# Performance work log

Measured on AMD Instinct MI355X. Metric: run time of the kernel, lower is better.

The kernel has to match this reference:

```python
import jax, jax.numpy as jnp
import numpy as np

EMBED_DIM = 768
HEAD_SIZE = 64

def setup_inputs() -> dict:
    key = jax.random.key(0)
    k1, k2, k3, k4 = jax.random.split(key, 4)
    x = jax.random.normal(k1, (4, 4096, EMBED_DIM), dtype=jnp.float32)
    # nn.Linear(E, H, bias=False) weights, stored as [E, H] for y = x @ W
    scale = 1.0 / np.sqrt(EMBED_DIM)
    Wk = jax.random.uniform(k2, (EMBED_DIM, HEAD_SIZE), jnp.float32, -scale, scale)
    Wq = jax.random.uniform(k3, (EMBED_DIM, HEAD_SIZE), jnp.float32, -scale, scale)
    Wv = jax.random.uniform(k4, (EMBED_DIM, HEAD_SIZE), jnp.float32, -scale, scale)
    return {"x": x, "Wk": Wk, "Wq": Wq, "Wv": Wv}

def reference(x, Wk, Wq, Wv):
    # x: [B, S, E]
    E = x.shape[2]
    K = jnp.einsum("bse,eh->bsh", x, Wk)  # [B, S, H]
    Q = jnp.einsum("bse,eh->bsh", x, Wq)
    V = jnp.einsum("bse,eh->bsh", x, Wv)
    # NOTE: original scales by embedding_dim**0.5, not head_size**0.5
    A = jnp.einsum("bqh,bkh->bqk", Q, K) / jnp.sqrt(jnp.asarray(E, x.dtype))
    A = jax.nn.softmax(A, axis=-1)
    # dropout is inference-mode identity
    return jnp.einsum("bqk,bkh->bqh", A, V)
```

## Files before the change

kernel.cpp:

```cpp
#include <hip/hip_runtime.h>

typedef __attribute__((ext_vector_type(8))) short short8;
typedef __attribute__((ext_vector_type(4))) short short4v;
typedef __attribute__((ext_vector_type(4))) float float4v;

__device__ __forceinline__ short f2bf(float f) {
    union { float f; unsigned u; } v; v.f = f;
    return (short)((v.u + 0x7fffu + ((v.u >> 16) & 1u)) >> 16);
}

__device__ __forceinline__ float fast_exp2(float x) {
#if __has_builtin(__builtin_amdgcn_exp2f)
    return __builtin_amdgcn_exp2f(x);
#else
    return exp2f(x);
#endif
}

__global__ void wtrans_kernel(const float* __restrict__ Wk, const float* __restrict__ Wq,
                              const float* __restrict__ Wv, short* __restrict__ Wt3) {
    int idx = blockIdx.x * 256 + threadIdx.x;
    int j = idx / (64 * 768);
    int rem = idx - j * (64 * 768);
    int n = rem / 768, k = rem - n * 768;
    const float* W = (j == 0) ? Wq : (j == 1 ? Wk : Wv);
    float scale = (j == 0) ? 0.05205877f : 1.0f;
    Wt3[idx] = f2bf(W[k * 64 + n] * scale);
}

__global__ __launch_bounds__(256, 4) void proj_kernel(
    const float* __restrict__ x, const short* __restrict__ Wt3,
    short* __restrict__ Qs, short* __restrict__ Kb, short* __restrict__ Vtr)
{
    __shared__ alignas(16) float red[3 * 64 * 48];
    const int tid = threadIdx.x;
    const int wave = tid >> 6, lane = tid & 63, quad = lane >> 4, l16 = lane & 15;
    const int m0 = blockIdx.x * 16;
    const int kb = wave * 192;
    const float* xr = x + (size_t)(m0 + l16) * 768 + kb + quad * 8;

    float4v acc[3][4];
#pragma unroll
    for (int j = 0; j < 3; ++j)
#pragma unroll
        for (int nt = 0; nt < 4; ++nt) acc[j][nt] = (float4v){0.f, 0.f, 0.f, 0.f};

#pragma unroll
    for (int it = 0; it < 6; ++it) {
        float4 u0 = *(const float4*)(xr + it * 32);
        float4 u1 = *(const float4*)(xr + it * 32 + 4);
        short8 a;
        a[0] = f2bf(u0.x); a[1] = f2bf(u0.y); a[2] = f2bf(u0.z); a[3] = f2bf(u0.w);
        a[4] = f2bf(u1.x); a[5] = f2bf(u1.y); a[6] = f2bf(u1.z); a[7] = f2bf(u1.w);
        const short* wb = Wt3 + kb + it * 32 + quad * 8;
#pragma unroll
        for (int j = 0; j < 3; ++j)
#pragma unroll
            for (int nt = 0; nt < 4; ++nt) {
                short8 bf = *(const short8*)(wb + (size_t)(j * 64 + nt * 16 + l16) * 768);
                acc[j][nt] = __builtin_amdgcn_mfma_f32_16x16x32_bf16(a, bf, acc[j][nt], 0, 0, 0);
            }
    }

    if (wave != 0) {
        float* dst = &red[((wave - 1) * 64 + lane) * 48];
#pragma unroll
        for (int j = 0; j < 3; ++j)
#pragma unroll
            for (int nt = 0; nt < 4; ++nt)
                *(float4v*)(dst + (j * 4 + nt) * 4) = acc[j][nt];
    }
    __syncthreads();
    if (wave == 0) {
#pragma unroll
        for (int w = 0; w < 3; ++w) {
            const float* srcp = &red[(w * 64 + lane) * 48];
#pragma unroll
            for (int j = 0; j < 3; ++j)
#pragma unroll
                for (int nt = 0; nt < 4; ++nt)
                    acc[j][nt] += *(const float4v*)(srcp + (j * 4 + nt) * 4);
        }
    }
    __syncthreads();

    short* sm = (short*)red;
    if (wave == 0) {
#pragma unroll
        for (int j = 0; j < 2; ++j) {
            short* dst = (j == 0) ? Qs : Kb;
#pragma unroll
            for (int nt = 0; nt < 4; ++nt)
#pragma unroll
                for (int r = 0; r < 4; ++r)
                    dst[(size_t)(m0 + quad * 4 + r) * 64 + nt * 16 + l16] = f2bf(acc[j][nt][r]);
        }
#pragma unroll
        for (int nt = 0; nt < 4; ++nt)
#pragma unroll
            for (int r = 0; r < 4; ++r)
                sm[(quad * 4 + r) * 72 + nt * 16 + l16] = f2bf(acc[2][nt][r]);
    }
    __syncthreads();
    {
        const int h = tid >> 2, si = (tid & 3) * 4;
        const int b = m0 >> 12, s0 = m0 & 4095;
        short4v tmp;
#pragma unroll
        for (int i = 0; i < 4; ++i) tmp[i] = sm[(si + i) * 72 + h];
        *(short4v*)(Vtr + (size_t)(b * 64 + h) * 4096 + s0 + si) = tmp;
    }
}

__global__ __launch_bounds__(256, 4) void attn_kernel(
    const short* __restrict__ Qs, const short* __restrict__ Kb, const short* __restrict__ Vt,
    float* __restrict__ Opart, float* __restrict__ Ll, int kv_len)
{
    __shared__ alignas(16) short Kl[64 * 72];
    __shared__ alignas(16) short Vl[64 * 72];
    __shared__ alignas(16) short Pl[4 * 32 * 72];

    const int tid = threadIdx.x;
    const int wave = tid >> 6, lane = tid & 63, quad = lane >> 4, l16 = lane & 15;
    const int qt = blockIdx.x, b = blockIdx.y, sp = blockIdx.z;
    const int q0 = qt * 128;
    const int bS = b * 4096;
    const int kv0 = sp * kv_len;

    short8 qa[2][2];
#pragma unroll
    for (int mt = 0; mt < 2; ++mt)
#pragma unroll
        for (int ks = 0; ks < 2; ++ks)
            qa[mt][ks] = *(const short8*)(Qs + (size_t)(bS + q0 + wave * 32 + mt * 16 + l16) * 64 + ks * 32 + quad * 8);

    float4v o[2][4];
    float rs[2][4];
#pragma unroll
    for (int mt = 0; mt < 2; ++mt)
#pragma unroll
        for (int nt = 0; nt < 4; ++nt) o[mt][nt] = (float4v){0.f, 0.f, 0.f, 0.f};
#pragma unroll
    for (int mt = 0; mt < 2; ++mt)
#pragma unroll
        for (int r = 0; r < 4; ++r) rs[mt][r] = 0.f;

    const int sr = tid >> 2, sc = (tid & 3) * 16;
    short* plw = &Pl[wave * 2304];

    for (int kt = 0; kt < kv_len; kt += 64) {
        const int kvg = kv0 + kt;
        __syncthreads();
        {
            const short* src = Kb + (size_t)(bS + kvg + sr) * 64 + sc;
            *(short8*)&Kl[sr * 72 + sc]     = *(const short8*)src;
            *(short8*)&Kl[sr * 72 + sc + 8] = *(const short8*)(src + 8);
            const short* vs = Vt + (size_t)(b * 64 + sr) * 4096 + kvg + sc;
            *(short8*)&Vl[sr * 72 + sc]     = *(const short8*)vs;
            *(short8*)&Vl[sr * 72 + sc + 8] = *(const short8*)(vs + 8);
        }
        __syncthreads();

        float4v s[2][4];
#pragma unroll
        for (int nt = 0; nt < 4; ++nt) {
            short8 b0 = *(const short8*)&Kl[(nt * 16 + l16) * 72 + quad * 8];
            short8 b1 = *(const short8*)&Kl[(nt * 16 + l16) * 72 + 32 + quad * 8];
#pragma unroll
            for (int mt = 0; mt < 2; ++mt) {
                float4v a0 = (float4v){0.f, 0.f, 0.f, 0.f};
                a0 = __builtin_amdgcn_mfma_f32_16x16x32_bf16(qa[mt][0], b0, a0, 0, 0, 0);
                a0 = __builtin_amdgcn_mfma_f32_16x16x32_bf16(qa[mt][1], b1, a0, 0, 0, 0);
                s[mt][nt] = a0;
            }
        }

#pragma unroll
        for (int mt = 0; mt < 2; ++mt)
#pragma unroll
            for (int nt = 0; nt < 4; ++nt)
#pragma unroll
                for (int r = 0; r < 4; ++r) {
                    float p = fast_exp2(s[mt][nt][r]);
                    rs[mt][r] += p;
                    plw[(mt * 16 + quad * 4 + r) * 72 + nt * 16 + l16] = f2bf(p);
                }

#pragma unroll
        for (int ks = 0; ks < 2; ++ks) {
            short8 bf[4];
#pragma unroll
            for (int nt = 0; nt < 4; ++nt)
                bf[nt] = *(const short8*)&Vl[(nt * 16 + l16) * 72 + ks * 32 + quad * 8];
#pragma unroll
            for (int mt = 0; mt < 2; ++mt) {
                short8 af = *(const short8*)&plw[(mt * 16 + l16) * 72 + ks * 32 + quad * 8];
#pragma unroll
                for (int nt = 0; nt < 4; ++nt)
                    o[mt][nt] = __builtin_amdgcn_mfma_f32_16x16x32_bf16(af, bf[nt], o[mt][nt], 0, 0, 0);
            }
        }
    }

#pragma unroll
    for (int mt = 0; mt < 2; ++mt)
#pragma unroll
        for (int r = 0; r < 4; ++r) {
#pragma unroll
            for (int off = 8; off >= 1; off >>= 1)
                rs[mt][r] += __shfl_xor(rs[mt][r], off);
        }

#pragma unroll
    for (int mt = 0; mt < 2; ++mt) {
#pragma unroll
        for (int nt = 0; nt < 4; ++nt)
#pragma unroll
            for (int r = 0; r < 4; ++r) {
                int qb = q0 + wave * 32 + mt * 16 + quad * 4 + r;
                Opart[((size_t)sp * 16384 + bS + qb) * 64 + nt * 16 + l16] = o[mt][nt][r];
            }
        if (l16 == 0) {
#pragma unroll
            for (int r = 0; r < 4; ++r) {
                int qb = q0 + wave * 32 + mt * 16 + quad * 4 + r;
                Ll[(size_t)sp * 16384 + bS + qb] = rs[mt][r];
            }
        }
    }
}

__global__ void combine_kernel(const float* __restrict__ Opart, const float* __restrict__ Ll,
                               float* __restrict__ out, int nsplit) {
    int idx = blockIdx.x * 256 + threadIdx.x;
    int q = idx >> 6;
    float den = 0.f, num = 0.f;
    for (int s = 0; s < nsplit; ++s) {
        den += Ll[s * 16384 + q];
        num += Opart[(size_t)s * 1048576 + idx];
    }
    out[idx] = num / den;
}

extern "C" void kernel_launch(void* const* d_in, const int* in_sizes, int n_in,
                              void* d_out, int out_size, void* d_ws, size_t ws_size,
                              hipStream_t stream) {
    const float* x  = (const float*)d_in[0];
    const float* Wk = (const float*)d_in[1];
    const float* Wq = (const float*)d_in[2];
    const float* Wv = (const float*)d_in[3];
    float* out = (float*)d_out;

    char* w = (char*)d_ws;
    size_t off = 0;
    auto take = [&](size_t bytes) -> void* {
        void* p = w + off;
        off = (off + bytes + 255) & ~(size_t)255;
        return p;
    };
    short* Qs  = (short*)take((size_t)16384 * 64 * 2);
    short* Kb  = (short*)take((size_t)16384 * 64 * 2);
    short* Vt  = (short*)take((size_t)16384 * 64 * 2);
    short* Wt3 = (short*)take((size_t)3 * 64 * 768 * 2);

    size_t base = off;
    int nsplit = 8;
    while (nsplit > 1) {
        size_t need = base + (((size_t)nsplit * 16384 * 4 + 255) & ~(size_t)255)
                      + (size_t)nsplit * 16384 * 64 * 4 + 512;
        if (need <= ws_size) break;
        nsplit >>= 1;
    }
    float* Ll    = (float*)take((size_t)nsplit * 16384 * 4);
    float* Opart = (float*)take((size_t)nsplit * 16384 * 64 * 4);

    wtrans_kernel<<<576, 256, 0, stream>>>(Wk, Wq, Wv, Wt3);
    proj_kernel<<<1024, 256, 0, stream>>>(x, Wt3, Qs, Kb, Vt);
    dim3 ag(32, 4, nsplit);
    attn_kernel<<<ag, 256, 0, stream>>>(Qs, Kb, Vt, Opart, Ll, 4096 / nsplit);
    combine_kernel<<<4096, 256, 0, stream>>>(Opart, Ll, out, nsplit);
}
```

Before: 163.0 us.

## Split projection across output tiles per wave with fragment-ordered weights and prefetch

The projection kernel previously split the K dimension across four waves and reduced partial accumulators through shared memory. Now each wave owns three output 16-column tiles over the full K range, which removes the LDS reduction and its barriers. Weights are pre-permuted into MFMA fragment order so each lane does one contiguous 16-byte load. A three-deep register prefetch of x and weight fragments hides load latency. Each wave now reads the whole x row strip, so x is loaded four times per block from cache instead of once, and the loop is longer.

```diff
diff --git a/kernel.cpp b/kernel.cpp
--- a/kernel.cpp
+++ b/kernel.cpp
@@ -18,88 +18,82 @@
 }
 
 __global__ void wtrans_kernel(const float* __restrict__ Wk, const float* __restrict__ Wq,
-                              const float* __restrict__ Wv, short* __restrict__ Wt3) {
+                              const float* __restrict__ Wv, short* __restrict__ Wt3T) {
     int idx = blockIdx.x * 256 + threadIdx.x;
-    int j = idx / (64 * 768);
-    int rem = idx - j * (64 * 768);
-    int n = rem / 768, k = rem - n * 768;
+    int p = idx / 12288;
+    int rem = idx - p * 12288;
+    int kstep = rem / 512;
+    int r2 = rem - kstep * 512;
+    int lane = r2 >> 3, i = r2 & 7;
+    int quad = lane >> 4, l16 = lane & 15;
+    int j = p >> 2, nt = p & 3;
+    int n = nt * 16 + l16;
+    int k = kstep * 32 + quad * 8 + i;
     const float* W = (j == 0) ? Wq : (j == 1 ? Wk : Wv);
     float scale = (j == 0) ? 0.05205877f : 1.0f;
-    Wt3[idx] = f2bf(W[k * 64 + n] * scale);
-}
-
-__global__ __launch_bounds__(256, 4) void proj_kernel(
-    const float* __restrict__ x, const short* __restrict__ Wt3,
+    Wt3T[idx] = f2bf(W[k * 64 + n] * scale);
+}
+
+__global__ __launch_bounds__(256) void proj_kernel(
+    const float* __restrict__ x, const short* __restrict__ Wt3T,
     short* __restrict__ Qs, short* __restrict__ Kb, short* __restrict__ Vtr)
 {
-    __shared__ alignas(16) float red[3 * 64 * 48];
+    __shared__ alignas(16) short sm[16 * 72];
     const int tid = threadIdx.x;
     const int wave = tid >> 6, lane = tid & 63, quad = lane >> 4, l16 = lane & 15;
     const int m0 = blockIdx.x * 16;
-    const int kb = wave * 192;
-    const float* xr = x + (size_t)(m0 + l16) * 768 + kb + quad * 8;
-
-    float4v acc[3][4];
-#pragma unroll
-    for (int j = 0; j < 3; ++j)
-#pragma unroll
-        for (int nt = 0; nt < 4; ++nt) acc[j][nt] = (float4v){0.f, 0.f, 0.f, 0.f};
-
-#pragma unroll
-    for (int it = 0; it < 6; ++it) {
-        float4 u0 = *(const float4*)(xr + it * 32);
-        float4 u1 = *(const float4*)(xr + it * 32 + 4);
+    const int p0 = wave * 3;
+    const float* xr = x + (size_t)(m0 + l16) * 768 + quad * 8;
+    const short* wt0 = Wt3T + (size_t)(p0 * 24) * 512 + lane * 8;
+
+    float4 X[3][2];
+    short8 Wf[3][3];
+#pragma unroll
+    for (int s = 0; s < 2; ++s) {
+        X[s][0] = *(const float4*)(xr + s * 32);
+        X[s][1] = *(const float4*)(xr + s * 32 + 4);
+#pragma unroll
+        for (int t = 0; t < 3; ++t)
+            Wf[s][t] = *(const short8*)(wt0 + t * 12288 + s * 512);
+    }
+
+    float4v acc[3];
+#pragma unroll
+    for (int t = 0; t < 3; ++t) acc[t] = (float4v){0.f, 0.f, 0.f, 0.f};
+
+#pragma unroll
+    for (int it = 0; it < 24; ++it) {
+        const int cur = it % 3, nxt = (it + 2) % 3;
+        if (it < 22) {
+            X[nxt][0] = *(const float4*)(xr + (it + 2) * 32);
+            X[nxt][1] = *(const float4*)(xr + (it + 2) * 32 + 4);
+#pragma unroll
+            for (int t = 0; t < 3; ++t)
+                Wf[nxt][t] = *(const short8*)(wt0 + t * 12288 + (it + 2) * 512);
+        }
         short8 a;
-        a[0] = f2bf(u0.x); a[1] = f2bf(u0.y); a[2] = f2bf(u0.z); a[3] = f2bf(u0.w);
-        a[4] = f2bf(u1.x); a[5] = f2bf(u1.y); a[6] = f2bf(u1.z); a[7] = f2bf(u1.w);
-        const short* wb = Wt3 + kb + it * 32 + quad * 8;
-#pragma unroll
-        for (int j = 0; j < 3; ++j)
-#pragma unroll
-            for (int nt = 0; nt < 4; ++nt) {
-                short8 bf = *(const short8*)(wb + (size_t)(j * 64 + nt * 16 + l16) * 768);
-                acc[j][nt] = __builtin_amdgcn_mfma_f32_16x16x32_bf16(a, bf, acc[j][nt], 0, 0, 0);
-            }
-    }
-
-    if (wave != 0) {
-        float* dst = &red[((wave - 1) * 64 + lane) * 48];
-#pragma unroll
-        for (int j = 0; j < 3; ++j)
-#pragma unroll
-            for (int nt = 0; nt < 4; ++nt)
-                *(float4v*)(dst + (j * 4 + nt) * 4) = acc[j][nt];
-    }
-    __syncthreads();
-    if (wave == 0) {
-#pragma unroll
-        for (int w = 0; w < 3; ++w) {
-            const float* srcp = &red[(w * 64 + lane) * 48];
-#pragma unroll
-            for (int j = 0; j < 3; ++j)
-#pragma unroll
-                for (int nt = 0; nt < 4; ++nt)
-                    acc[j][nt] += *(const float4v*)(srcp + (j * 4 + nt) * 4);
-        }
-    }
-    __syncthreads();
-
-    short* sm = (short*)red;
-    if (wave == 0) {
-#pragma unroll
-        for (int j = 0; j < 2; ++j) {
+        a[0] = f2bf(X[cur][0].x); a[1] = f2bf(X[cur][0].y);
+        a[2] = f2bf(X[cur][0].z); a[3] = f2bf(X[cur][0].w);
+        a[4] = f2bf(X[cur][1].x); a[5] = f2bf(X[cur][1].y);
+        a[6] = f2bf(X[cur][1].z); a[7] = f2bf(X[cur][1].w);
+#pragma unroll
+        for (int t = 0; t < 3; ++t)
+            acc[t] = __builtin_amdgcn_mfma_f32_16x16x32_bf16(a, Wf[cur][t], acc[t], 0, 0, 0);
+    }
+
+#pragma unroll
+    for (int t = 0; t < 3; ++t) {
+        const int p = p0 + t, j = p >> 2, nt = p & 3;
+        if (j < 2) {
             short* dst = (j == 0) ? Qs : Kb;
 #pragma unroll
-            for (int nt = 0; nt < 4; ++nt)
-#pragma unroll
-                for (int r = 0; r < 4; ++r)
-                    dst[(size_t)(m0 + quad * 4 + r) * 64 + nt * 16 + l16] = f2bf(acc[j][nt][r]);
-        }
-#pragma unroll
-        for (int nt = 0; nt < 4; ++nt)
-#pragma unroll
             for (int r = 0; r < 4; ++r)
-                sm[(quad * 4 + r) * 72 + nt * 16 + l16] = f2bf(acc[2][nt][r]);
+                dst[(size_t)(m0 + quad * 4 + r) * 64 + nt * 16 + l16] = f2bf(acc[t][r]);
+        } else {
+#pragma unroll
+            for (int r = 0; r < 4; ++r)
+                sm[(quad * 4 + r) * 72 + nt * 16 + l16] = f2bf(acc[t][r]);
+        }
     }
     __syncthreads();
     {
```

Result: faster. 154.1 us (-5.5%).
